# Optimization experiments

Measured on AMD Instinct MI355X. Metric: run time of the kernel, lower is better.

The kernel has to match this reference:

```python
import jax, jax.numpy as jnp
import numpy as np

NUM_HEADS = 16
HEAD_DIM = 64
HIDDEN = NUM_HEADS * HEAD_DIM
LN_EPS = 1e-6


def setup_inputs() -> dict:
    key = jax.random.key(0)
    ks = jax.random.split(key, 5)
    B, T, H = 2, 2048, HIDDEN
    s = 1.0 / np.sqrt(H)
    return {
        "h": jax.random.normal(ks[0], (B, T, H), jnp.float32),
        "Wq": jax.random.normal(ks[1], (H, H), jnp.float32) * s,
        "bq": jnp.zeros((H,), jnp.float32),
        "Wk": jax.random.normal(ks[2], (H, H), jnp.float32) * s,
        "bk": jnp.zeros((H,), jnp.float32),
        "Wv": jax.random.normal(ks[3], (H, H), jnp.float32) * s,
        "bv": jnp.zeros((H,), jnp.float32),
        "Wo": jax.random.normal(ks[4], (H, H), jnp.float32) * s,
        "bo": jnp.zeros((H,), jnp.float32),
        "gamma": jnp.ones((H,), jnp.float32),
        "beta": jnp.zeros((H,), jnp.float32),
    }


def _split_heads(x):
    B, T, H = x.shape
    return x.reshape(B, T, NUM_HEADS, HEAD_DIM).transpose(0, 2, 1, 3)  # [B,h,T,d]


def reference(h, Wq, bq, Wk, bk, Wv, bv, Wo, bo, gamma, beta):
    # QKV projections (nn.Linear: x @ W^T + b)
    Q = _split_heads(h @ Wq.T + bq)
    K = _split_heads(h @ Wk.T + bk)
    V = _split_heads(h @ Wv.T + bv)
    scale = HEAD_DIM ** -0.5
    scores = jnp.einsum("bhqd,bhkd->bhqk", Q, K) * scale  # [B,h,T,T]
    attn = jax.nn.softmax(scores, axis=-1)
    ctx = jnp.einsum("bhqk,bhkd->bhqd", attn, V)          # [B,h,T,d]
    B, _, T, _ = ctx.shape
    ctx = ctx.transpose(0, 2, 1, 3).reshape(B, T, HIDDEN)
    out = ctx @ Wo.T + bo + h  # dropout is identity at eval
    # LayerNorm(eps=1e-6)
    mu = out.mean(-1, keepdims=True)
    var = jnp.mean((out - mu) ** 2, -1, keepdims=True)
    return (out - mu) * jax.lax.rsqrt(var + LN_EPS) * gamma + beta
```

## Files before the change

kernel.cpp:

```cpp
#include <hip/hip_runtime.h>
#include <hip/hip_bf16.h>

#define NH   16
#define HD   64
#define HID  1024
#define TSEQ 2048
#define BATCH 2
#define KSCALE 0.18033688011112042f

typedef __attribute__((ext_vector_type(4))) float f32x4;
typedef __attribute__((ext_vector_type(8))) short s16x8;
typedef __attribute__((ext_vector_type(4))) short s16x4;
typedef __attribute__((ext_vector_type(8))) _Float16 f16x8;
typedef __attribute__((ext_vector_type(4))) _Float16 f16x4;
typedef __attribute__((ext_vector_type(2))) _Float16 f16x2;

__device__ __forceinline__ unsigned short f2bf(float f) {
  union { float f; unsigned int u; } v; v.f = f;
  unsigned int r = v.u + 0x7fffu + ((v.u >> 16) & 1u);
  return (unsigned short)(r >> 16);
}
__device__ __forceinline__ float bf2f(unsigned short b) {
  union { unsigned int u; float f; } v; v.u = ((unsigned int)b) << 16; return v.f;
}

__device__ __forceinline__ void gll16(const void* g, void* l) {
  __builtin_amdgcn_global_load_lds(
      (const __attribute__((address_space(1))) unsigned int*)g,
      (__attribute__((address_space(3))) unsigned int*)l, 16, 0, 0);
}

#define WAITBAR(N)                                                      \
  do {                                                                  \
    __builtin_amdgcn_sched_barrier(0);                                  \
    asm volatile("s_waitcnt vmcnt(" #N ")\n\ts_barrier" ::: "memory");  \
  } while (0)

__global__ __launch_bounds__(256) void cast_all_k(
    const float* __restrict__ h,
    const float* __restrict__ w0, const float* __restrict__ w1,
    const float* __restrict__ w2, const float* __restrict__ w3,
    unsigned short* __restrict__ hb, unsigned short* __restrict__ wbase) {
  int i = blockIdx.x * 256 + threadIdx.x;
  const float* src; unsigned short* dst; int idx; float sc = 1.f;
  if (i < 1048576) { src = h; dst = hb; idx = i; }
  else {
    int idx4 = i - 1048576;
    int w = idx4 >> 18;
    idx = idx4 & 262143;
    src = (w == 0) ? w0 : (w == 1) ? w1 : (w == 2) ? w2 : w3;
    dst = wbase + (size_t)(idx4 - idx) * 4;
    if (w == 1) sc = KSCALE;
  }
  float4 v = ((const float4*)src)[idx];
  ushort4 o;
  o.x = f2bf(v.x * sc); o.y = f2bf(v.y * sc); o.z = f2bf(v.z * sc); o.w = f2bf(v.w * sc);
  ((ushort4*)dst)[idx] = o;
}

__global__ __launch_bounds__(256) void gemm_qkv(
    const unsigned short* __restrict__ hb,
    const unsigned short* __restrict__ wcat,
    const float* __restrict__ bq, const float* __restrict__ bk, const float* __restrict__ bv,
    unsigned short* __restrict__ qo, unsigned short* __restrict__ ko,
    unsigned short* __restrict__ vto) {
  __shared__ unsigned short Ash[3][128 * 32];
  __shared__ unsigned short Bsh[3][128 * 32];
  const int tid = threadIdx.x, lane = tid & 63, wave = tid >> 6;
  const int l15 = lane & 15, quad = lane >> 4;
  const int wr = wave >> 1, wc = wave & 1;
  const int bn = blockIdx.x * 128, bm = blockIdx.y * 128;
  const char* Ab = (const char*)(hb + (size_t)bm * HID);
  const char* Bb = (const char*)(wcat + (size_t)bn * HID);
  const int off = tid * 16;
  const int r0 = off >> 6;
  const int q0i = (off >> 4) & 3;
  const int c0 = (q0i ^ (r0 & 3)) << 4;
  const size_t ga0 = (size_t)r0 * (HID * 2) + c0;
  const size_t ga1 = ga0 + (size_t)64 * (HID * 2);
  const int lb0 = wave * 512;
  const int lb1 = 2048 + wave * 512;

  f32x4 acc[4][4];
#pragma unroll
  for (int i = 0; i < 4; ++i)
#pragma unroll
    for (int j = 0; j < 4; ++j) acc[i][j] = f32x4{0.f, 0.f, 0.f, 0.f};

  auto stage = [&](int bufi, int k0) {
    const size_t kb = (size_t)k0 * 2;
    gll16(Ab + ga0 + kb, &Ash[bufi][lb0]);
    gll16(Ab + ga1 + kb, &Ash[bufi][lb1]);
    gll16(Bb + ga0 + kb, &Bsh[bufi][lb0]);
    gll16(Bb + ga1 + kb, &Bsh[bufi][lb1]);
  };
  const int qx = (quad ^ (l15 & 3)) * 8;
  auto compute = [&](int bufi) {
    s16x8 af[4], bfr[4];
#pragma unroll
    for (int i = 0; i < 4; ++i)
      af[i] = *(const s16x8*)(&Ash[bufi][(wr * 64 + i * 16 + l15) * 32 + qx]);
#pragma unroll
    for (int j = 0; j < 4; ++j)
      bfr[j] = *(const s16x8*)(&Bsh[bufi][(wc * 64 + j * 16 + l15) * 32 + qx]);
#pragma unroll
    for (int i = 0; i < 4; ++i)
#pragma unroll
      for (int j = 0; j < 4; ++j)
        acc[i][j] = __builtin_amdgcn_mfma_f32_16x16x32_bf16(af[i], bfr[j], acc[i][j], 0, 0, 0);
  };

  stage(0, 0);
  stage(1, 32);
  int cur = 0, pf = 2;
  const int NT = HID / 32;
  for (int t = 0; t < NT - 1; ++t) {
    WAITBAR(4);
    if (t + 2 < NT) stage(pf, (t + 2) * 32);
    compute(cur);
    cur = (cur == 2) ? 0 : cur + 1;
    pf  = (pf  == 2) ? 0 : pf + 1;
  }
  WAITBAR(0);
  compute(cur);

  const int mat = bn >> 10;
  const int cb = (bn & 1023) + wc * 64;
  const int rbase = bm + wr * 64;
  if (mat == 2) {
#pragma unroll
    for (int j = 0; j < 4; ++j) {
      const int coln = cb + j * 16 + l15;
      const int head = coln >> 6, d = coln & 63;
      const float bb = bv[coln];
#pragma unroll
      for (int i = 0; i < 4; ++i) {
        const int row0 = rbase + i * 16 + quad * 4;
        const int bI = row0 >> 11, t0 = row0 & 2047;
        unsigned short o[4];
#pragma unroll
        for (int r = 0; r < 4; ++r) {
          _Float16 hv = (_Float16)(acc[i][j][r] + bb);
          o[r] = __builtin_bit_cast(unsigned short, hv);
        }
        *(s16x4*)(vto + ((size_t)((bI * NH + head) * HD + d)) * TSEQ + t0) = *(const s16x4*)o;
      }
    }
  } else {
    unsigned short* dst = (mat == 0) ? qo : ko;
#pragma unroll
    for (int j = 0; j < 4; ++j) {
      const int coln = cb + j * 16 + l15;
      const int head = coln >> 6, d = coln & 63;
      const float bb = (mat == 0) ? bq[coln] : bk[coln] * KSCALE;
#pragma unroll
      for (int i = 0; i < 4; ++i) {
#pragma unroll
        for (int r = 0; r < 4; ++r) {
          const int row = rbase + i * 16 + quad * 4 + r;
          const int bI = row >> 11, t = row & 2047;
          dst[(((size_t)(bI * NH + head) * TSEQ) + t) * HD + d] = f2bf(acc[i][j][r] + bb);
        }
      }
    }
  }
}

__global__ __launch_bounds__(256) void gemm_out(
    const unsigned short* __restrict__ ctx, const unsigned short* __restrict__ wo,
    const float* __restrict__ bo, const float* __restrict__ hres,
    float* __restrict__ outf) {
  __shared__ unsigned short Ash[3][128 * 32];
  __shared__ unsigned short Bsh[3][64 * 32];
  const int tid = threadIdx.x, lane = tid & 63, wave = tid >> 6;
  const int l15 = lane & 15, quad = lane >> 4;
  const int wr = wave >> 1, wc = wave & 1;
  const int bn = blockIdx.x * 64, bm = blockIdx.y * 128;
  const char* Ab = (const char*)(ctx + (size_t)bm * HID);
  const char* Bb = (const char*)(wo + (size_t)bn * HID);
  const int off = tid * 16;
  const int r0 = off >> 6;
  const int q0i = (off >> 4) & 3;
  const int c0 = (q0i ^ (r0 & 3)) << 4;
  const size_t ga0 = (size_t)r0 * (HID * 2) + c0;
  const size_t ga1 = ga0 + (size_t)64 * (HID * 2);
  const int lb0 = wave * 512, lb1 = 2048 + wave * 512;

  f32x4 acc[4][2];
#pragma unroll
  for (int i = 0; i < 4; ++i)
#pragma unroll
    for (int j = 0; j < 2; ++j) acc[i][j] = f32x4{0.f, 0.f, 0.f, 0.f};

  auto stage = [&](int bufi, int k0) {
    const size_t kb = (size_t)k0 * 2;
    gll16(Ab + ga0 + kb, &Ash[bufi][lb0]);
    gll16(Ab + ga1 + kb, &Ash[bufi][lb1]);
    gll16(Bb + ga0 + kb, &Bsh[bufi][lb0]);
  };
  const int qx = (quad ^ (l15 & 3)) * 8;
  auto compute = [&](int bufi) {
    s16x8 af[4], bfr[2];
#pragma unroll
    for (int i = 0; i < 4; ++i)
      af[i] = *(const s16x8*)(&Ash[bufi][(wr * 64 + i * 16 + l15) * 32 + qx]);
#pragma unroll
    for (int j = 0; j < 2; ++j)
      bfr[j] = *(const s16x8*)(&Bsh[bufi][(wc * 32 + j * 16 + l15) * 32 + qx]);
#pragma unroll
    for (int i = 0; i < 4; ++i)
#pragma unroll
      for (int j = 0; j < 2; ++j)
        acc[i][j] = __builtin_amdgcn_mfma_f32_16x16x32_bf16(af[i], bfr[j], acc[i][j], 0, 0, 0);
  };

  stage(0, 0);
  stage(1, 32);
  int cur = 0, pf = 2;
  const int NT = HID / 32;
  for (int t = 0; t < NT - 1; ++t) {
    WAITBAR(3);
    if (t + 2 < NT) stage(pf, (t + 2) * 32);
    compute(cur);
    cur = (cur == 2) ? 0 : cur + 1;
    pf  = (pf  == 2) ? 0 : pf + 1;
  }
  WAITBAR(0);
  compute(cur);

#pragma unroll
  for (int j = 0; j < 2; ++j) {
    const int col = bn + wc * 32 + j * 16 + l15;
    const float bb = bo[col];
#pragma unroll
    for (int i = 0; i < 4; ++i) {
#pragma unroll
      for (int r = 0; r < 4; ++r) {
        const int row = bm + wr * 64 + i * 16 + quad * 4 + r;
        const size_t o = (size_t)row * HID + col;
        outf[o] = acc[i][j][r] + bb + hres[o];
      }
    }
  }
}

__global__ __launch_bounds__(256, 2) void attn_k(
    const unsigned short* __restrict__ qb, const unsigned short* __restrict__ kb,
    const unsigned short* __restrict__ vt, unsigned short* __restrict__ ctx,
    unsigned short* __restrict__ Opart, float* __restrict__ rsumP,
    int lsplit, int ntiles) {
  __shared__ unsigned short Ksh[64 * 72];
  __shared__ unsigned short Vsh[64 * 72];

  const int tid = threadIdx.x, lane = tid & 63, wave = tid >> 6;
  const int l15 = lane & 15, quad = lane >> 4;
  const int z = blockIdx.z;
  const int b = z >> lsplit;
  const int part = z & ((1 << lsplit) - 1);
  const int h = blockIdx.y, qt = blockIdx.x;
  const size_t ho = ((size_t)(b * NH + h)) * TSEQ * HD;
  const unsigned short* Qh = qb + ho;
  const unsigned short* Kh = kb + ho;
  const unsigned short* Vh = vt + ho;
  const int q0 = qt * 128 + wave * 32;
  const int kt0 = part * ntiles;

  s16x8 qf[2][2];
#pragma unroll
  for (int s = 0; s < 2; ++s)
#pragma unroll
    for (int ks = 0; ks < 2; ++ks)
      qf[s][ks] = *(const s16x8*)(Qh + (size_t)(q0 + s * 16 + l15) * HD + ks * 32 + quad * 8);

  f32x4 accO[4][2];
  float rsum[2];
#pragma unroll
  for (int n2 = 0; n2 < 4; ++n2)
#pragma unroll
    for (int s = 0; s < 2; ++s) accO[n2][s] = f32x4{0.f, 0.f, 0.f, 0.f};
  rsum[0] = rsum[1] = 0.f;

  const int sr = tid >> 3, sc = (tid & 7) * 8;
  s16x8 kreg[2], vreg[2];
#pragma unroll
  for (int hf = 0; hf < 2; ++hf) {
    kreg[hf] = *(const s16x8*)(Kh + (size_t)(kt0 * 64 + sr + hf * 32) * HD + sc);
    vreg[hf] = *(const s16x8*)(Vh + (size_t)(sr + hf * 32) * TSEQ + kt0 * 64 + sc);
  }

  for (int kt = 0; kt < ntiles; ++kt) {
    __syncthreads();
#pragma unroll
    for (int hf = 0; hf < 2; ++hf) {
      *(s16x8*)(Ksh + (sr + hf * 32) * 72 + sc) = kreg[hf];
      *(s16x8*)(Vsh + (sr + hf * 32) * 72 + sc) = vreg[hf];
    }
    __syncthreads();
    if (kt + 1 < ntiles) {
      const int k0n = (kt0 + kt + 1) * 64;
#pragma unroll
      for (int hf = 0; hf < 2; ++hf) {
        kreg[hf] = *(const s16x8*)(Kh + (size_t)(k0n + sr + hf * 32) * HD + sc);
        vreg[hf] = *(const s16x8*)(Vh + (size_t)(sr + hf * 32) * TSEQ + k0n + sc);
      }
    }

    f32x4 accS[2][4];
#pragma unroll
    for (int s = 0; s < 2; ++s)
#pragma unroll
      for (int n = 0; n < 4; ++n) accS[s][n] = f32x4{0.f, 0.f, 0.f, 0.f};
#pragma unroll
    for (int ks = 0; ks < 2; ++ks) {
#pragma unroll
      for (int n = 0; n < 4; ++n) {
        s16x8 kf = *(const s16x8*)(Ksh + (n * 16 + l15) * 72 + ks * 32 + quad * 8);
#pragma unroll
        for (int s = 0; s < 2; ++s)
          accS[s][n] = __builtin_amdgcn_mfma_f32_16x16x32_bf16(kf, qf[s][ks], accS[s][n], 0, 0, 0);
      }
    }

    f16x4 pB[2][4];
#pragma unroll
    for (int s = 0; s < 2; ++s)
#pragma unroll
      for (int n = 0; n < 4; ++n) {
        float e0 = __builtin_amdgcn_exp2f(accS[s][n][0]);
        float e1 = __builtin_amdgcn_exp2f(accS[s][n][1]);
        float e2 = __builtin_amdgcn_exp2f(accS[s][n][2]);
        float e3 = __builtin_amdgcn_exp2f(accS[s][n][3]);
        rsum[s] += (e0 + e1) + (e2 + e3);
        f16x2 lo = __builtin_bit_cast(f16x2, __builtin_amdgcn_cvt_pkrtz(e0, e1));
        f16x2 hi = __builtin_bit_cast(f16x2, __builtin_amdgcn_cvt_pkrtz(e2, e3));
        pB[s][n] = f16x4{lo[0], lo[1], hi[0], hi[1]};
      }

#pragma unroll
    for (int n = 0; n < 4; ++n) {
#pragma unroll
      for (int n2 = 0; n2 < 4; ++n2) {
        f16x4 vA = *(const f16x4*)(Vsh + (n2 * 16 + l15) * 72 + n * 16 + quad * 4);
#pragma unroll
        for (int s = 0; s < 2; ++s)
          accO[n2][s] = __builtin_amdgcn_mfma_f32_16x16x16f16(vA, pB[s][n], accO[n2][s], 0, 0, 0);
      }
    }
  }

#pragma unroll
  for (int s = 0; s < 2; ++s) {
    float t = rsum[s];
    t += __shfl_xor(t, 16, 64);
    t += __shfl_xor(t, 32, 64);
    rsum[s] = t;
  }

  if (lsplit) {
    const int slot = (part * BATCH + b) * NH + h;
    const size_t ob = (size_t)slot * TSEQ * HD;
#pragma unroll
    for (int s = 0; s < 2; ++s) {
      const int t = q0 + s * 16 + l15;
#pragma unroll
      for (int n2 = 0; n2 < 4; ++n2) {
        const int d0 = n2 * 16 + quad * 4;
        unsigned short o[4];
#pragma unroll
        for (int r = 0; r < 4; ++r) o[r] = f2bf(accO[n2][s][r]);
        *(s16x4*)(Opart + ob + (size_t)t * HD + d0) = *(const s16x4*)o;
      }
    }
    if (quad == 0) {
      const size_t rb = (size_t)slot * TSEQ;
#pragma unroll
      for (int s = 0; s < 2; ++s)
        rsumP[rb + q0 + s * 16 + l15] = rsum[s];
    }
  } else {
#pragma unroll
    for (int s = 0; s < 2; ++s) {
      const int t = q0 + s * 16 + l15;
      const float inv = 1.f / rsum[s];
#pragma unroll
      for (int n2 = 0; n2 < 4; ++n2) {
        const int d0 = n2 * 16 + quad * 4;
        unsigned short o[4];
#pragma unroll
        for (int r = 0; r < 4; ++r) o[r] = f2bf(accO[n2][s][r] * inv);
        *(s16x4*)(ctx + ((size_t)(b * TSEQ + t)) * HID + h * HD + d0) = *(const s16x4*)o;
      }
    }
  }
}

__global__ __launch_bounds__(256) void combine_k(
    const unsigned short* __restrict__ Opart, const float* __restrict__ rsumP,
    unsigned short* __restrict__ ctx, int nparts) {
  const int gtid = blockIdx.x * 256 + threadIdx.x;
  const int d = (gtid & 7) * 8;
  const int rem = gtid >> 3;
  const int t = rem & 2047;
  const int bh = rem >> 11;
  float acc[8] = {0, 0, 0, 0, 0, 0, 0, 0};
  float rs = 0.f;
  for (int p = 0; p < nparts; ++p) {
    const int slot = p * 32 + bh;
    s16x8 a = *(const s16x8*)(Opart + ((size_t)slot * TSEQ + t) * HD + d);
#pragma unroll
    for (int j = 0; j < 8; ++j) acc[j] += bf2f(((const unsigned short*)&a)[j]);
    rs += rsumP[(size_t)slot * TSEQ + t];
  }
  const float inv = 1.f / rs;
  unsigned short o[8];
#pragma unroll
  for (int j = 0; j < 8; ++j) o[j] = f2bf(acc[j] * inv);
  const int b = bh >> 4, h = bh & 15;
  *(s16x8*)(ctx + ((size_t)(b * TSEQ + t)) * HID + h * HD + d) = *(const s16x8*)o;
}

__global__ __launch_bounds__(256) void ln_k(float* __restrict__ io,
                                            const float* __restrict__ gamma,
                                            const float* __restrict__ beta) {
  const int row = blockIdx.x, tid = threadIdx.x;
  float x[4]; float s = 0.f, s2 = 0.f;
#pragma unroll
  for (int i = 0; i < 4; ++i) {
    x[i] = io[(size_t)row * HID + tid + i * 256];
    s += x[i]; s2 += x[i] * x[i];
  }
#pragma unroll
  for (int off = 1; off < 64; off <<= 1) {
    s  += __shfl_xor(s, off, 64);
    s2 += __shfl_xor(s2, off, 64);
  }
  __shared__ float red[8];
  const int wave = tid >> 6;
  if ((tid & 63) == 0) { red[wave] = s; red[wave + 4] = s2; }
  __syncthreads();
  s  = red[0] + red[1] + red[2] + red[3];
  s2 = red[4] + red[5] + red[6] + red[7];
  const float mean = s * (1.f / HID);
  const float var  = s2 * (1.f / HID) - mean * mean;
  const float rstd = rsqrtf(var + 1e-6f);
#pragma unroll
  for (int i = 0; i < 4; ++i) {
    const int col = tid + i * 256;
    io[(size_t)row * HID + col] = (x[i] - mean) * rstd * gamma[col] + beta[col];
  }
}

extern "C" void kernel_launch(void* const* d_in, const int* in_sizes, int n_in,
                              void* d_out, int out_size, void* d_ws, size_t ws_size,
                              hipStream_t stream) {
  const float* h    = (const float*)d_in[0];
  const float* Wq   = (const float*)d_in[1];
  const float* bq   = (const float*)d_in[2];
  const float* Wk   = (const float*)d_in[3];
  const float* bk   = (const float*)d_in[4];
  const float* Wv   = (const float*)d_in[5];
  const float* bv   = (const float*)d_in[6];
  const float* Wo   = (const float*)d_in[7];
  const float* bo   = (const float*)d_in[8];
  const float* gamma = (const float*)d_in[9];
  const float* beta  = (const float*)d_in[10];
  float* out = (float*)d_out;

  unsigned short* hb   = (unsigned short*)d_ws;
  unsigned short* wqb  = hb  + 4194304;
  unsigned short* wkb  = wqb + 1048576;
  unsigned short* wvb  = wkb + 1048576;
  unsigned short* wob  = wvb + 1048576;
  unsigned short* qb   = wob + 1048576;
  unsigned short* kb   = qb  + 4194304;
  unsigned short* vtf  = kb  + 4194304;
  unsigned short* Opart = vtf + 4194304;
  unsigned short* ctxb = hb;

  const size_t base = (size_t)(vtf + 4194304 - hb) * 2;
  int lsplit = 0;
  if (ws_size >= base + 2u * 8388608 + 2u * 262144) lsplit = 1;
  const int nparts = 1 << lsplit;
  float* rsumP = (float*)(Opart + (size_t)nparts * 4194304);

  cast_all_k<<<8192, 256, 0, stream>>>(h, Wq, Wk, Wv, Wo, hb, wqb);
  gemm_qkv<<<dim3(24, 32), 256, 0, stream>>>(hb, wqb, bq, bk, bv, qb, kb, vtf);
  attn_k<<<dim3(TSEQ / 128, NH, BATCH << lsplit), 256, 0, stream>>>(
      qb, kb, vtf, ctxb, Opart, rsumP, lsplit, 32 >> lsplit);
  if (lsplit)
    combine_k<<<2048, 256, 0, stream>>>(Opart, rsumP, ctxb, nparts);
  gemm_out<<<dim3(16, 32), 256, 0, stream>>>(ctxb, wob, bo, h, out);
  ln_k<<<4096, 256, 0, stream>>>(out, gamma, beta);
}
```

Measured before the change: 234.9 us.

## Deepen GEMM LDS pipeline to five stages and drop XOR swizzle

Both projection GEMMs go from a 3-buffer, 2-ahead prefetch ring to a 5-buffer, 4-ahead ring, with the wait counts and the drain tail adjusted to match. The aim is to hide more global-load latency behind MFMA work. The XOR swizzle on LDS stores and fragment reads is removed and replaced by a linear layout. That may bring back LDS bank conflicts on the 16-byte fragment reads, and the larger LDS footprint can lower occupancy.

```diff
diff --git a/kernel.cpp b/kernel.cpp
--- a/kernel.cpp
+++ b/kernel.cpp
@@ -64,8 +64,8 @@
     const float* __restrict__ bq, const float* __restrict__ bk, const float* __restrict__ bv,
     unsigned short* __restrict__ qo, unsigned short* __restrict__ ko,
     unsigned short* __restrict__ vto) {
-  __shared__ unsigned short Ash[3][128 * 32];
-  __shared__ unsigned short Bsh[3][128 * 32];
+  __shared__ unsigned short Ash[5][128 * 32];
+  __shared__ unsigned short Bsh[5][128 * 32];
   const int tid = threadIdx.x, lane = tid & 63, wave = tid >> 6;
   const int l15 = lane & 15, quad = lane >> 4;
   const int wr = wave >> 1, wc = wave & 1;
@@ -73,9 +73,7 @@
   const char* Ab = (const char*)(hb + (size_t)bm * HID);
   const char* Bb = (const char*)(wcat + (size_t)bn * HID);
   const int off = tid * 16;
-  const int r0 = off >> 6;
-  const int q0i = (off >> 4) & 3;
-  const int c0 = (q0i ^ (r0 & 3)) << 4;
+  const int r0 = off >> 6, c0 = off & 63;
   const size_t ga0 = (size_t)r0 * (HID * 2) + c0;
   const size_t ga1 = ga0 + (size_t)64 * (HID * 2);
   const int lb0 = wave * 512;
@@ -94,15 +92,14 @@
     gll16(Bb + ga0 + kb, &Bsh[bufi][lb0]);
     gll16(Bb + ga1 + kb, &Bsh[bufi][lb1]);
   };
-  const int qx = (quad ^ (l15 & 3)) * 8;
   auto compute = [&](int bufi) {
     s16x8 af[4], bfr[4];
 #pragma unroll
     for (int i = 0; i < 4; ++i)
-      af[i] = *(const s16x8*)(&Ash[bufi][(wr * 64 + i * 16 + l15) * 32 + qx]);
+      af[i] = *(const s16x8*)(&Ash[bufi][(wr * 64 + i * 16 + l15) * 32 + quad * 8]);
 #pragma unroll
     for (int j = 0; j < 4; ++j)
-      bfr[j] = *(const s16x8*)(&Bsh[bufi][(wc * 64 + j * 16 + l15) * 32 + qx]);
+      bfr[j] = *(const s16x8*)(&Bsh[bufi][(wc * 64 + j * 16 + l15) * 32 + quad * 8]);
 #pragma unroll
     for (int i = 0; i < 4; ++i)
 #pragma unroll
@@ -112,17 +109,21 @@
 
   stage(0, 0);
   stage(1, 32);
-  int cur = 0, pf = 2;
+  stage(2, 64);
+  stage(3, 96);
+  int cur = 0, pf = 4;
   const int NT = HID / 32;
-  for (int t = 0; t < NT - 1; ++t) {
-    WAITBAR(4);
-    if (t + 2 < NT) stage(pf, (t + 2) * 32);
+  for (int t = 0; t < NT - 4; ++t) {
+    WAITBAR(12);
+    stage(pf, (t + 4) * 32);
     compute(cur);
-    cur = (cur == 2) ? 0 : cur + 1;
-    pf  = (pf  == 2) ? 0 : pf + 1;
-  }
-  WAITBAR(0);
-  compute(cur);
+    cur = (cur == 4) ? 0 : cur + 1;
+    pf  = (pf  == 4) ? 0 : pf + 1;
+  }
+  WAITBAR(12); compute(cur); cur = (cur == 4) ? 0 : cur + 1;
+  WAITBAR(8);  compute(cur); cur = (cur == 4) ? 0 : cur + 1;
+  WAITBAR(4);  compute(cur); cur = (cur == 4) ? 0 : cur + 1;
+  WAITBAR(0);  compute(cur);
 
   const int mat = bn >> 10;
   const int cb = (bn & 1023) + wc * 64;
@@ -170,8 +171,8 @@
     const unsigned short* __restrict__ ctx, const unsigned short* __restrict__ wo,
     const float* __restrict__ bo, const float* __restrict__ hres,
     float* __restrict__ outf) {
-  __shared__ unsigned short Ash[3][128 * 32];
-  __shared__ unsigned short Bsh[3][64 * 32];
+  __shared__ unsigned short Ash[5][128 * 32];
+  __shared__ unsigned short Bsh[5][64 * 32];
   const int tid = threadIdx.x, lane = tid & 63, wave = tid >> 6;
   const int l15 = lane & 15, quad = lane >> 4;
   const int wr = wave >> 1, wc = wave & 1;
@@ -179,9 +180,7 @@
   const char* Ab = (const char*)(ctx + (size_t)bm * HID);
   const char* Bb = (const char*)(wo + (size_t)bn * HID);
   const int off = tid * 16;
-  const int r0 = off >> 6;
-  const int q0i = (off >> 4) & 3;
-  const int c0 = (q0i ^ (r0 & 3)) << 4;
+  const int r0 = off >> 6, c0 = off & 63;
   const size_t ga0 = (size_t)r0 * (HID * 2) + c0;
   const size_t ga1 = ga0 + (size_t)64 * (HID * 2);
   const int lb0 = wave * 512, lb1 = 2048 + wave * 512;
@@ -198,15 +197,14 @@
     gll16(Ab + ga1 + kb, &Ash[bufi][lb1]);
     gll16(Bb + ga0 + kb, &Bsh[bufi][lb0]);
   };
-  const int qx = (quad ^ (l15 & 3)) * 8;
   auto compute = [&](int bufi) {
     s16x8 af[4], bfr[2];
 #pragma unroll
     for (int i = 0; i < 4; ++i)
-      af[i] = *(const s16x8*)(&Ash[bufi][(wr * 64 + i * 16 + l15) * 32 + qx]);
+      af[i] = *(const s16x8*)(&Ash[bufi][(wr * 64 + i * 16 + l15) * 32 + quad * 8]);
 #pragma unroll
     for (int j = 0; j < 2; ++j)
-      bfr[j] = *(const s16x8*)(&Bsh[bufi][(wc * 32 + j * 16 + l15) * 32 + qx]);
+      bfr[j] = *(const s16x8*)(&Bsh[bufi][(wc * 32 + j * 16 + l15) * 32 + quad * 8]);
 #pragma unroll
     for (int i = 0; i < 4; ++i)
 #pragma unroll
@@ -216,17 +214,21 @@
 
   stage(0, 0);
   stage(1, 32);
-  int cur = 0, pf = 2;
+  stage(2, 64);
+  stage(3, 96);
+  int cur = 0, pf = 4;
   const int NT = HID / 32;
-  for (int t = 0; t < NT - 1; ++t) {
-    WAITBAR(3);
-    if (t + 2 < NT) stage(pf, (t + 2) * 32);
+  for (int t = 0; t < NT - 4; ++t) {
+    WAITBAR(9);
+    stage(pf, (t + 4) * 32);
     compute(cur);
-    cur = (cur == 2) ? 0 : cur + 1;
-    pf  = (pf  == 2) ? 0 : pf + 1;
-  }
-  WAITBAR(0);
-  compute(cur);
+    cur = (cur == 4) ? 0 : cur + 1;
+    pf  = (pf  == 4) ? 0 : pf + 1;
+  }
+  WAITBAR(9); compute(cur); cur = (cur == 4) ? 0 : cur + 1;
+  WAITBAR(6); compute(cur); cur = (cur == 4) ? 0 : cur + 1;
+  WAITBAR(3); compute(cur); cur = (cur == 4) ? 0 : cur + 1;
+  WAITBAR(0); compute(cur);
 
 #pragma unroll
   for (int j = 0; j < 2; ++j) {
```

New measurement: 221.3 us. 1.06x faster.
